# Kernel optimization log

Measured on AMD Instinct MI355X. Metric: run time of the kernel, lower is better.

## Reference

```python
import jax, jax.numpy as jnp
import numpy as np

N_NODES = 100000
N_EDGES = 1600000
N_CLASS = 10
HIDDEN = 128
BN_EPS = 1e-5


def _bn(h, gamma, beta):
    # BatchNorm1d in training mode: biased batch statistics over the node dim
    m = h.mean(axis=0)
    v = ((h - m) ** 2).mean(axis=0)
    return gamma * (h - m) / jnp.sqrt(v + BN_EPS) + beta


def _mlp(h, w1, b1, g1, t1, w2, b2, g2, t2):
    h = jax.nn.relu(_bn(h @ w1 + b1, g1, t1))
    h = jax.nn.relu(_bn(h @ w2 + b2, g2, t2))
    return h


def _gin_conv(x, edge_index, mlp_params):
    src, dst = edge_index[0], edge_index[1]
    # sum-aggregate neighbor messages: [E, D] gather + scatter-add -> [N, D]
    agg = jax.ops.segment_sum(x[src], dst, num_segments=N_NODES)
    h = x + agg  # (1 + eps) * x + agg, eps = 0
    return _mlp(h, *mlp_params)


def setup_inputs() -> dict:
    key = jax.random.key(0)
    ks = jax.random.split(key, 16)
    x = jax.random.normal(ks[0], (N_NODES, N_CLASS), dtype=jnp.float32)
    edge_index = jax.random.randint(ks[1], (2, N_EDGES), 0, N_NODES, dtype=jnp.int64)
    edge_weight = jax.random.uniform(ks[2], (N_EDGES,), dtype=jnp.float32)

    def lin(k, fan_in, fan_out):
        bound = 1.0 / np.sqrt(fan_in)
        kw, kb = jax.random.split(k)
        w = jax.random.uniform(kw, (fan_in, fan_out), minval=-bound, maxval=bound, dtype=jnp.float32)
        b = jax.random.uniform(kb, (fan_out,), minval=-bound, maxval=bound, dtype=jnp.float32)
        return w, b

    w11, b11 = lin(ks[3], N_CLASS, HIDDEN)
    w12, b12 = lin(ks[4], HIDDEN, HIDDEN)
    w21, b21 = lin(ks[5], HIDDEN, HIDDEN)
    w22, b22 = lin(ks[6], HIDDEN, HIDDEN)
    wf, bf = lin(ks[7], HIDDEN, N_CLASS)
    ones = jnp.ones((HIDDEN,), jnp.float32)
    zeros = jnp.zeros((HIDDEN,), jnp.float32)
    return {
        "x": x, "edge_weight": edge_weight,
        "w11": w11, "b11": b11, "g11": ones, "t11": zeros,
        "w12": w12, "b12": b12, "g12": ones, "t12": zeros,
        "w21": w21, "b21": b21, "g21": ones, "t21": zeros,
        "w22": w22, "b22": b22, "g22": ones, "t22": zeros,
        "wf": wf, "bf": bf,
        "edge_index": edge_index,
    }


def reference(x, edge_weight, w11, b11, g11, t11, w12, b12, g12, t12,
              w21, b21, g21, t21, w22, b22, g22, t22, wf, bf, edge_index):
    h = jax.nn.relu(_gin_conv(x, edge_index, (w11, b11, g11, t11, w12, b12, g12, t12)))
    h = jax.nn.relu(_gin_conv(h, edge_index, (w21, b21, g21, t21, w22, b22, g22, t22)))
    logits = h @ wf + bf
    return jax.nn.log_softmax(logits, axis=1)
```

## Files before the change

### kernel.cpp

```cpp
#include <hip/hip_runtime.h>

#define N_CLASS 10
#define HIDDEN 128
#define BN_EPS 1e-5f

typedef short short8 __attribute__((ext_vector_type(8)));
typedef float floatx4 __attribute__((ext_vector_type(4)));

__device__ __forceinline__ float bf2f(unsigned short u) {
    unsigned int x = ((unsigned int)u) << 16;
    float f; __builtin_memcpy(&f, &x, 4); return f;
}
__device__ __forceinline__ unsigned short f2bf(float f) {
    unsigned int x; __builtin_memcpy(&x, &f, 4);
    x += 0x7FFFu + ((x >> 16) & 1u);
    return (unsigned short)(x >> 16);
}
__device__ __forceinline__ float lo_f(unsigned int u) {
    unsigned int x = u << 16; float f; __builtin_memcpy(&f, &x, 4); return f;
}
__device__ __forceinline__ float hi_f(unsigned int u) {
    unsigned int x = u & 0xffff0000u; float f; __builtin_memcpy(&f, &x, 4); return f;
}

__global__ void hist_k(const int* __restrict__ ei, int* __restrict__ cnt,
                       int* __restrict__ rank, int E) {
    int e = blockIdx.x * 256 + threadIdx.x;
    if (e < E) rank[e] = atomicAdd(cnt + ei[E + e], 1);
}

__global__ void scanA_k(const int* __restrict__ cnt, int* __restrict__ bsum, int N) {
    __shared__ int sm[256];
    int i = blockIdx.x * 256 + threadIdx.x;
    sm[threadIdx.x] = (i < N) ? cnt[i] : 0;
    __syncthreads();
    for (int s = 128; s > 0; s >>= 1) {
        if (threadIdx.x < s) sm[threadIdx.x] += sm[threadIdx.x + s];
        __syncthreads();
    }
    if (threadIdx.x == 0) bsum[blockIdx.x] = sm[0];
}

__global__ void scanB_k(int* __restrict__ bsum, int B) {
    __shared__ int sm[512];
    int t = threadIdx.x;
    sm[t] = (t < B) ? bsum[t] : 0;
    __syncthreads();
    for (int off = 1; off < 512; off <<= 1) {
        int u = (t >= off) ? sm[t - off] : 0;
        __syncthreads();
        sm[t] += u;
        __syncthreads();
    }
    if (t < B) bsum[t] = (t == 0) ? 0 : sm[t - 1];
}

__global__ void scanC_k(const int* __restrict__ cnt, const int* __restrict__ boff,
                        int* __restrict__ row_ptr, int N) {
    __shared__ int sm[256];
    int i = blockIdx.x * 256 + threadIdx.x;
    int t = threadIdx.x;
    int v = (i < N) ? cnt[i] : 0;
    sm[t] = v;
    __syncthreads();
    for (int off = 1; off < 256; off <<= 1) {
        int u = (t >= off) ? sm[t - off] : 0;
        __syncthreads();
        sm[t] += u;
        __syncthreads();
    }
    if (i < N) row_ptr[i] = boff[blockIdx.x] + sm[t] - v;
}

__global__ void fill_k(const int* __restrict__ ei, const int* __restrict__ rank,
                       const int* __restrict__ rp, int* __restrict__ col,
                       int E, int N) {
    const int P = 4;
    const int rs = (N + P - 1) / P;
    const int stride = gridDim.x * 256;
#pragma unroll 1
    for (int pass = 0; pass < P; ++pass) {
        int lo = pass * rs, hi = lo + rs;
        for (int e = blockIdx.x * 256 + threadIdx.x; e < E; e += stride) {
            int d = ei[E + e];
            if (d >= lo && d < hi)
                col[rp[d] + rank[e]] = ei[e];
        }
    }
}

__global__ void prep_k(const float* __restrict__ W0, const float* __restrict__ W1,
                       const float* __restrict__ W2,
                       unsigned short* __restrict__ T0, unsigned short* __restrict__ T1,
                       unsigned short* __restrict__ T2,
                       float* __restrict__ stats, int* __restrict__ cnt, int N) {
    const float* W = (blockIdx.y == 0) ? W0 : (blockIdx.y == 1) ? W1 : W2;
    unsigned short* T = (blockIdx.y == 0) ? T0 : (blockIdx.y == 1) ? T1 : T2;
    int i = blockIdx.x * 256 + threadIdx.x;
    if (i < 128 * 128) {
        int k = i >> 7, n = i & 127;
        T[n * 128 + k] = f2bf(W[k * 128 + n]);
    }
    if (blockIdx.y == 0) {
        if (i < 1024) stats[i] = 0.f;
        for (int c = i; c < N; c += 64 * 256) cnt[c] = 0;
    }
}

__global__ void padx_k(const float* __restrict__ X, float* __restrict__ XP, int N) {
    int i = blockIdx.x * 256 + threadIdx.x;
    if (i >= N * 16) return;
    int node = i >> 4, f = i & 15;
    XP[i] = (f < N_CLASS) ? X[node * N_CLASS + f] : 0.f;
}

__global__ void gather10_k(const float* __restrict__ XP, const int* __restrict__ col,
                           const int* __restrict__ rp, const int* __restrict__ cnt,
                           float* __restrict__ out, int N) {
    int t = blockIdx.x * 256 + threadIdx.x;
    int node = t >> 4, f = t & 15;
    if (node >= N) return;
    int start = rp[node], deg = cnt[node];
    float acc = XP[node * 16 + f];
    int j = 0;
    for (; j + 8 <= deg; j += 8) {
        int s0 = col[start + j],     s1 = col[start + j + 1];
        int s2 = col[start + j + 2], s3 = col[start + j + 3];
        int s4 = col[start + j + 4], s5 = col[start + j + 5];
        int s6 = col[start + j + 6], s7 = col[start + j + 7];
        float v0 = XP[s0 * 16 + f];
        float v1 = XP[s1 * 16 + f];
        float v2 = XP[s2 * 16 + f];
        float v3 = XP[s3 * 16 + f];
        float v4 = XP[s4 * 16 + f];
        float v5 = XP[s5 * 16 + f];
        float v6 = XP[s6 * 16 + f];
        float v7 = XP[s7 * 16 + f];
        acc += v0; acc += v1; acc += v2; acc += v3;
        acc += v4; acc += v5; acc += v6; acc += v7;
    }
    for (; j < deg; ++j)
        acc += XP[col[start + j] * 16 + f];
    out[node * 16 + f] = acc;
}

__global__ __launch_bounds__(256) void act2_k(
    const unsigned short* __restrict__ Z, unsigned short* __restrict__ R,
    const float* __restrict__ st, const float* __restrict__ g,
    const float* __restrict__ b, int N, float inv_n) {
    __shared__ float sTab[128], hTab[128];
    int tid = threadIdx.x;
    if (tid < 128) {
        float m = st[tid] * inv_n;
        float v = fmaxf(st[128 + tid] * inv_n - m * m, 0.f);
        float s = g[tid] * rsqrtf(v + BN_EPS);
        sTab[tid] = s;
        hTab[tid] = b[tid] - m * s;
    }
    __syncthreads();
    int total = N * 16;
    for (int i = blockIdx.x * 256 + tid; i < total; i += gridDim.x * 256) {
        int k8 = (i & 15) * 8;
        uint4 v = ((const uint4*)Z)[i];
        unsigned short* us = (unsigned short*)&v;
#pragma unroll
        for (int j = 0; j < 8; ++j) {
            float f = fmaxf(fmaf(bf2f(us[j]), sTab[k8 + j], hTab[k8 + j]), 0.f);
            us[j] = f2bf(f);
        }
        ((uint4*)R)[i] = v;
    }
}

__global__ __launch_bounds__(256) void gather_sum_k(
    const unsigned short* __restrict__ R, const int* __restrict__ col,
    const int* __restrict__ rp, const int* __restrict__ cnt,
    unsigned short* __restrict__ out, int N) {
    int wave = __builtin_amdgcn_readfirstlane((blockIdx.x * 256 + threadIdx.x) >> 6);
    int lane = threadIdx.x & 63;
    if (wave >= N) return;
    int start = __builtin_amdgcn_readfirstlane(rp[wave]);
    int deg   = __builtin_amdgcn_readfirstlane(cnt[wave]);
    const unsigned int* Xv = (const unsigned int*)R;
    unsigned int self = Xv[wave * 64 + lane];
    float a0 = lo_f(self);
    float a1 = hi_f(self);
    int j = 0;
    for (; j + 8 <= deg; j += 8) {
        int n0 = col[start + j],     n1 = col[start + j + 1];
        int n2 = col[start + j + 2], n3 = col[start + j + 3];
        int n4 = col[start + j + 4], n5 = col[start + j + 5];
        int n6 = col[start + j + 6], n7 = col[start + j + 7];
        unsigned int w0 = Xv[n0 * 64 + lane];
        unsigned int w1 = Xv[n1 * 64 + lane];
        unsigned int w2 = Xv[n2 * 64 + lane];
        unsigned int w3 = Xv[n3 * 64 + lane];
        unsigned int w4 = Xv[n4 * 64 + lane];
        unsigned int w5 = Xv[n5 * 64 + lane];
        unsigned int w6 = Xv[n6 * 64 + lane];
        unsigned int w7 = Xv[n7 * 64 + lane];
        a0 += lo_f(w0); a1 += hi_f(w0);
        a0 += lo_f(w1); a1 += hi_f(w1);
        a0 += lo_f(w2); a1 += hi_f(w2);
        a0 += lo_f(w3); a1 += hi_f(w3);
        a0 += lo_f(w4); a1 += hi_f(w4);
        a0 += lo_f(w5); a1 += hi_f(w5);
        a0 += lo_f(w6); a1 += hi_f(w6);
        a0 += lo_f(w7); a1 += hi_f(w7);
    }
    for (; j < deg; ++j) {
        unsigned int v = Xv[col[start + j] * 64 + lane];
        a0 += lo_f(v); a1 += hi_f(v);
    }
    unsigned int o = (unsigned int)f2bf(a0) | ((unsigned int)f2bf(a1) << 16);
    ((unsigned int*)out)[wave * 64 + lane] = o;
}

__global__ __launch_bounds__(128) void gemm10_k(
    const float* __restrict__ A, const float* __restrict__ W,
    const float* __restrict__ bias, unsigned short* __restrict__ C,
    float* __restrict__ stOut, int N) {
    __shared__ float rb[16 * 16];
    const int tid = threadIdx.x;
    float wreg[N_CLASS];
#pragma unroll
    for (int k = 0; k < N_CLASS; ++k) wreg[k] = W[k * HIDDEN + tid];
    float bb = bias[tid];
    float s = 0.f, s2 = 0.f;
    for (int r0 = blockIdx.x * 16; r0 < N; r0 += gridDim.x * 16) {
        int nr = min(16, N - r0);
        for (int i = tid; i < nr * 16; i += 128) rb[i] = A[r0 * 16 + i];
        __syncthreads();
        for (int r = 0; r < nr; ++r) {
            float acc = bb;
#pragma unroll
            for (int k = 0; k < N_CLASS; ++k) acc = fmaf(rb[r * 16 + k], wreg[k], acc);
            C[(r0 + r) * HIDDEN + tid] = f2bf(acc);
            s += acc; s2 += acc * acc;
        }
        __syncthreads();
    }
    atomicAdd(stOut + tid, s);
    atomicAdd(stOut + HIDDEN + tid, s2);
}

template<bool BN>
__global__ __launch_bounds__(256) void gemm_mfma_k(
    const unsigned short* __restrict__ Zin, const unsigned short* __restrict__ Wt,
    const float* __restrict__ bias,
    const float* __restrict__ stIn, const float* __restrict__ gIn,
    const float* __restrict__ tIn,
    unsigned short* __restrict__ Zout, float* __restrict__ stOut,
    int N, float inv_n) {
    __shared__ unsigned short Wl[128 * 136];
    __shared__ unsigned short Al[64 * 136];
    __shared__ float sTab[128], hTab[128], biasTab[128];
    __shared__ float redS[128], redS2[128];

    const int tid  = threadIdx.x;
    const int wv   = tid >> 6;
    const int ln   = tid & 63;
    const int half = ln >> 4;
    const int l16  = ln & 15;

    if (tid < 128) {
        biasTab[tid] = bias[tid];
        if (BN) {
            float m = stIn[tid] * inv_n;
            float v = fmaxf(stIn[128 + tid] * inv_n - m * m, 0.f);
            float s = gIn[tid] * rsqrtf(v + BN_EPS);
            sTab[tid] = s;
            hTab[tid] = tIn[tid] - m * s;
        }
        redS[tid] = 0.f; redS2[tid] = 0.f;
    }
    for (int c = tid; c < 2048; c += 256) {
        int n = c >> 4, k8 = c & 15;
        uint4 v = *(const uint4*)(Wt + n * 128 + k8 * 8);
        *(uint4*)(&Wl[n * 136 + k8 * 8]) = v;
    }
    __syncthreads();

    float cs[8], cs2[8];
#pragma unroll
    for (int i = 0; i < 8; ++i) { cs[i] = 0.f; cs2[i] = 0.f; }

    const int ntiles = (N + 63) >> 6;
    for (int tile = blockIdx.x; tile < ntiles; tile += gridDim.x) {
        const int r0 = tile * 64;
        for (int c = tid; c < 1024; c += 256) {
            int r = c >> 4, k8 = c & 15;
            int gr = r0 + r; if (gr >= N) gr = N - 1;
            uint4 v = *(const uint4*)(Zin + gr * 128 + k8 * 8);
            if (BN) {
                unsigned short* us = (unsigned short*)&v;
                int kb = k8 * 8;
#pragma unroll
                for (int j = 0; j < 8; ++j) {
                    float f = fmaxf(fmaf(bf2f(us[j]), sTab[kb + j], hTab[kb + j]), 0.f);
                    us[j] = f2bf(f);
                }
            }
            *(uint4*)(&Al[r * 136 + k8 * 8]) = v;
        }
        __syncthreads();

        short8 afrag[4];
        const int arow = wv * 16 + l16;
#pragma unroll
        for (int s = 0; s < 4; ++s)
            afrag[s] = *(const short8*)(&Al[arow * 136 + s * 32 + half * 8]);
        __syncthreads();

#pragma unroll
        for (int ct = 0; ct < 8; ++ct) {
            floatx4 acc = {0.f, 0.f, 0.f, 0.f};
            const int bn_ = ct * 16 + l16;
#pragma unroll
            for (int s = 0; s < 4; ++s) {
                short8 bfrag = *(const short8*)(&Wl[bn_ * 136 + s * 32 + half * 8]);
                acc = __builtin_amdgcn_mfma_f32_16x16x32_bf16(afrag[s], bfrag, acc, 0, 0, 0);
            }
            float bcol = biasTab[bn_];
#pragma unroll
            for (int r = 0; r < 4; ++r) {
                int lrow = wv * 16 + half * 4 + r;
                float val = acc[r] + bcol;
                if (r0 + lrow < N) { cs[ct] += val; cs2[ct] += val * val; }
                Al[lrow * 136 + bn_] = f2bf(val);
            }
        }
        __syncthreads();

        for (int c = tid; c < 1024; c += 256) {
            int r = c >> 4, k8 = c & 15;
            int gr = r0 + r;
            if (gr < N)
                *(uint4*)(Zout + gr * 128 + k8 * 8) = *(const uint4*)(&Al[r * 136 + k8 * 8]);
        }
        __syncthreads();
    }

#pragma unroll
    for (int ct = 0; ct < 8; ++ct) {
        float a = cs[ct], b = cs2[ct];
        a += __shfl_xor(a, 16); a += __shfl_xor(a, 32);
        b += __shfl_xor(b, 16); b += __shfl_xor(b, 32);
        if (half == 0) {
            atomicAdd(&redS[ct * 16 + l16], a);
            atomicAdd(&redS2[ct * 16 + l16], b);
        }
    }
    __syncthreads();
    if (tid < 128) {
        atomicAdd(stOut + tid, redS[tid]);
        atomicAdd(stOut + 128 + tid, redS2[tid]);
    }
}

__global__ __launch_bounds__(256) void final_mfma_k(
    const unsigned short* __restrict__ Z, const float* __restrict__ st,
    const float* __restrict__ g, const float* __restrict__ b,
    const float* __restrict__ wf, const float* __restrict__ bfc,
    float* __restrict__ out, int N, float inv_n) {
    __shared__ unsigned short Al[64 * 136];
    __shared__ unsigned short Bl[16 * 136];
    __shared__ float sTab[128], hTab[128], biasTab[16];

    const int tid  = threadIdx.x;
    const int wv   = tid >> 6;
    const int ln   = tid & 63;
    const int half = ln >> 4;
    const int l16  = ln & 15;

    if (tid < 128) {
        float m = st[tid] * inv_n;
        float v = fmaxf(st[128 + tid] * inv_n - m * m, 0.f);
        float s = g[tid] * rsqrtf(v + BN_EPS);
        sTab[tid] = s;
        hTab[tid] = b[tid] - m * s;
    }
    if (tid < 16) biasTab[tid] = (tid < N_CLASS) ? bfc[tid] : -3.0e38f;
    {
        int n = tid >> 4, k8 = (tid & 15) * 8;
        uint4 v;
        unsigned short* us = (unsigned short*)&v;
#pragma unroll
        for (int j = 0; j < 8; ++j)
            us[j] = (n < N_CLASS) ? f2bf(wf[(k8 + j) * N_CLASS + n]) : (unsigned short)0;
        *(uint4*)(&Bl[n * 136 + k8]) = v;
    }
    __syncthreads();

    short8 bfrag[4];
#pragma unroll
    for (int s = 0; s < 4; ++s)
        bfrag[s] = *(const short8*)(&Bl[l16 * 136 + s * 32 + half * 8]);

    const int ntiles = (N + 63) >> 6;
    for (int tile = blockIdx.x; tile < ntiles; tile += gridDim.x) {
        const int r0 = tile * 64;
        for (int c = tid; c < 1024; c += 256) {
            int r = c >> 4, k8 = c & 15;
            int gr = r0 + r; if (gr >= N) gr = N - 1;
            uint4 v = *(const uint4*)(Z + gr * 128 + k8 * 8);
            unsigned short* us = (unsigned short*)&v;
            int kb = k8 * 8;
#pragma unroll
            for (int j = 0; j < 8; ++j) {
                float f = fmaxf(fmaf(bf2f(us[j]), sTab[kb + j], hTab[kb + j]), 0.f);
                us[j] = f2bf(f);
            }
            *(uint4*)(&Al[r * 136 + k8 * 8]) = v;
        }
        __syncthreads();

        short8 afrag[4];
        const int arow = wv * 16 + l16;
#pragma unroll
        for (int s = 0; s < 4; ++s)
            afrag[s] = *(const short8*)(&Al[arow * 136 + s * 32 + half * 8]);
        __syncthreads();

        floatx4 acc = {0.f, 0.f, 0.f, 0.f};
#pragma unroll
        for (int s = 0; s < 4; ++s)
            acc = __builtin_amdgcn_mfma_f32_16x16x32_bf16(afrag[s], bfrag[s], acc, 0, 0, 0);

        float bcol = biasTab[l16];
#pragma unroll
        for (int r = 0; r < 4; ++r) {
            float lg = acc[r] + bcol;
            float mx = lg;
            mx = fmaxf(mx, __shfl_xor(mx, 1));
            mx = fmaxf(mx, __shfl_xor(mx, 2));
            mx = fmaxf(mx, __shfl_xor(mx, 4));
            mx = fmaxf(mx, __shfl_xor(mx, 8));
            float p = __expf(lg - mx);
            float se = p;
            se += __shfl_xor(se, 1);
            se += __shfl_xor(se, 2);
            se += __shfl_xor(se, 4);
            se += __shfl_xor(se, 8);
            float ls = __logf(se);
            int grow = r0 + wv * 16 + half * 4 + r;
            if (l16 < N_CLASS && grow < N)
                out[grow * N_CLASS + l16] = lg - mx - ls;
        }
    }
}


extern "C" void kernel_launch(void* const* d_in, const int* in_sizes, int n_in,
                              void* d_out, int out_size, void* d_ws, size_t ws_size,
                              hipStream_t stream) {
    const float* x   = (const float*)d_in[0];
    const float* w11 = (const float*)d_in[2];
    const float* b11 = (const float*)d_in[3];
    const float* g11 = (const float*)d_in[4];
    const float* t11 = (const float*)d_in[5];
    const float* w12 = (const float*)d_in[6];
    const float* b12 = (const float*)d_in[7];
    const float* g12 = (const float*)d_in[8];
    const float* t12 = (const float*)d_in[9];
    const float* w21 = (const float*)d_in[10];
    const float* b21 = (const float*)d_in[11];
    const float* g21 = (const float*)d_in[12];
    const float* t21 = (const float*)d_in[13];
    const float* w22 = (const float*)d_in[14];
    const float* b22 = (const float*)d_in[15];
    const float* g22 = (const float*)d_in[16];
    const float* t22 = (const float*)d_in[17];
    const float* wf  = (const float*)d_in[18];
    const float* bf  = (const float*)d_in[19];
    const int*   ei  = (const int*)d_in[20];

    const int N = in_sizes[0] / N_CLASS;
    const int E = in_sizes[1];
    const float inv_n = 1.0f / (float)N;

    char* base = (char*)d_ws;
    size_t off = 0;
    auto take = [&](size_t bytes) { void* p = base + off; off += (bytes + 15) & ~(size_t)15; return p; };
    float*          stats   = (float*)take(1024 * 4);
    float*          xp      = (float*)take((size_t)N * 16 * 4);
    float*          h0      = (float*)take((size_t)N * 16 * 4);
    int*            cnt     = (int*)take((size_t)N * 4);
    int*            row_ptr = (int*)take((size_t)N * 4);
    int*            rank    = (int*)take((size_t)E * 4);
    int*            bsum    = (int*)take(512 * 4);
    int*            col     = (int*)take((size_t)E * 4);
    unsigned short* bufA    = (unsigned short*)take((size_t)N * HIDDEN * 2);
    unsigned short* bufB    = (unsigned short*)take((size_t)N * HIDDEN * 2);
    unsigned short* bufC    = (unsigned short*)take((size_t)N * HIDDEN * 2);
    unsigned short* Wt1     = (unsigned short*)take(128 * 128 * 2);
    unsigned short* Wt2     = (unsigned short*)take(128 * 128 * 2);
    unsigned short* Wt3     = (unsigned short*)take(128 * 128 * 2);

    const int nB = (N + 255) / 256;
    const int gE = (E + 255) / 256;

    prep_k<<<dim3(64, 3), 256, 0, stream>>>(w12, w21, w22, Wt1, Wt2, Wt3,
                                            stats, cnt, N);
    padx_k<<<(N * 16 + 255) / 256, 256, 0, stream>>>(x, xp, N);

    hist_k<<<gE, 256, 0, stream>>>(ei, cnt, rank, E);
    scanA_k<<<nB, 256, 0, stream>>>(cnt, bsum, N);
    scanB_k<<<1, 512, 0, stream>>>(bsum, nB);
    scanC_k<<<nB, 256, 0, stream>>>(cnt, bsum, row_ptr, N);
    fill_k<<<gE, 256, 0, stream>>>(ei, rank, row_ptr, col, E, N);

    gather10_k<<<(N * 16 + 255) / 256, 256, 0, stream>>>(xp, col, row_ptr, cnt, h0, N);
    gemm10_k<<<512, 128, 0, stream>>>(h0, w11, b11, bufA, stats, N);
    gemm_mfma_k<true><<<512, 256, 0, stream>>>(bufA, Wt1, b12, stats, g11, t11,
                                               bufB, stats + 256, N, inv_n);

    act2_k<<<3125, 256, 0, stream>>>(bufB, bufC, stats + 256, g12, t12, N, inv_n);
    gather_sum_k<<<(N * 64 + 255) / 256, 256, 0, stream>>>(bufC, col, row_ptr, cnt,
                                                           bufA, N);

    gemm_mfma_k<false><<<512, 256, 0, stream>>>(bufA, Wt2, b21, nullptr, nullptr, nullptr,
                                                bufB, stats + 512, N, inv_n);
    gemm_mfma_k<true><<<512, 256, 0, stream>>>(bufB, Wt3, b22, stats + 512, g21, t21,
                                               bufA, stats + 768, N, inv_n);

    final_mfma_k<<<782, 256, 0, stream>>>(bufA, stats + 768, g22, t22,
                                          wf, bf, (float*)d_out, N, inv_n);
}
```

Before: 434.9 us.

## Build CSR via two-level bucket sort with shared-memory atomics

```diff
diff --git a/kernel.cpp b/kernel.cpp
--- a/kernel.cpp
+++ b/kernel.cpp
@@ -23,28 +23,25 @@
     unsigned int x = u & 0xffff0000u; float f; __builtin_memcpy(&f, &x, 4); return f;
 }
 
-__global__ void hist_k(const int* __restrict__ ei, int* __restrict__ cnt,
-                       int* __restrict__ rank, int E) {
-    int e = blockIdx.x * 256 + threadIdx.x;
-    if (e < E) rank[e] = atomicAdd(cnt + ei[E + e], 1);
-}
-
-__global__ void scanA_k(const int* __restrict__ cnt, int* __restrict__ bsum, int N) {
-    __shared__ int sm[256];
-    int i = blockIdx.x * 256 + threadIdx.x;
-    sm[threadIdx.x] = (i < N) ? cnt[i] : 0;
-    __syncthreads();
-    for (int s = 128; s > 0; s >>= 1) {
-        if (threadIdx.x < s) sm[threadIdx.x] += sm[threadIdx.x + s];
-        __syncthreads();
-    }
-    if (threadIdx.x == 0) bsum[blockIdx.x] = sm[0];
-}
-
-__global__ void scanB_k(int* __restrict__ bsum, int B) {
+
+__global__ __launch_bounds__(512) void bhist_k(const int* __restrict__ ei,
+                                               int* __restrict__ bhist, int E) {
+    __shared__ int h[512];
+    int tid = threadIdx.x;
+    h[tid] = 0;
+    __syncthreads();
+    for (int e = blockIdx.x * 512 + tid; e < E; e += gridDim.x * 512)
+        atomicAdd(&h[((unsigned)ei[E + e]) >> 8], 1);
+    __syncthreads();
+    if (h[tid]) atomicAdd(&bhist[tid], h[tid]);
+}
+
+__global__ __launch_bounds__(512) void bscan_k(const int* __restrict__ bhist,
+                                               int* __restrict__ bstart,
+                                               int* __restrict__ bcur, int NBK) {
     __shared__ int sm[512];
     int t = threadIdx.x;
-    sm[t] = (t < B) ? bsum[t] : 0;
+    sm[t] = (t < NBK) ? bhist[t] : 0;
     __syncthreads();
     for (int off = 1; off < 512; off <<= 1) {
         int u = (t >= off) ? sm[t - off] : 0;
@@ -52,40 +49,67 @@
         sm[t] += u;
         __syncthreads();
     }
-    if (t < B) bsum[t] = (t == 0) ? 0 : sm[t - 1];
-}
-
-__global__ void scanC_k(const int* __restrict__ cnt, const int* __restrict__ boff,
-                        int* __restrict__ row_ptr, int N) {
-    __shared__ int sm[256];
-    int i = blockIdx.x * 256 + threadIdx.x;
-    int t = threadIdx.x;
-    int v = (i < N) ? cnt[i] : 0;
-    sm[t] = v;
+    int excl = (t == 0) ? 0 : sm[t - 1];
+    if (t <= NBK) bstart[t] = excl;
+    if (t < NBK)  bcur[t]   = excl;
+}
+
+__global__ __launch_bounds__(512) void bscatter_k(const int* __restrict__ ei,
+                                                  int* __restrict__ bcur,
+                                                  int2* __restrict__ pairs, int E) {
+    __shared__ int h[512], base[512], cur[512];
+    int tid = threadIdx.x;
+    h[tid] = 0; cur[tid] = 0;
+    __syncthreads();
+    int chunk = (E + gridDim.x - 1) / gridDim.x;
+    int e0 = blockIdx.x * chunk;
+    int e1 = min(e0 + chunk, E);
+    for (int e = e0 + tid; e < e1; e += 512)
+        atomicAdd(&h[((unsigned)ei[E + e]) >> 8], 1);
+    __syncthreads();
+    base[tid] = h[tid] ? atomicAdd(&bcur[tid], h[tid]) : 0;
+    __syncthreads();
+    for (int e = e0 + tid; e < e1; e += 512) {
+        int s = ei[e], d = ei[E + e];
+        int bk = ((unsigned)d) >> 8;
+        int r = atomicAdd(&cur[bk], 1);
+        pairs[base[bk] + r] = make_int2(s, d);
+    }
+}
+
+__global__ __launch_bounds__(512) void bcsr_k(const int2* __restrict__ pairs,
+                                              const int* __restrict__ bstart,
+                                              int* __restrict__ row_ptr,
+                                              int* __restrict__ cnt,
+                                              int* __restrict__ col, int N) {
+    __shared__ int h[256], sc[256], cur[256];
+    int tid = threadIdx.x;
+    if (tid < 256) { h[tid] = 0; cur[tid] = 0; }
+    __syncthreads();
+    int b = blockIdx.x, lo = b << 8;
+    int s = bstart[b], e = bstart[b + 1];
+    for (int i = s + tid; i < e; i += 512)
+        atomicAdd(&h[pairs[i].y - lo], 1);
+    __syncthreads();
+    if (tid < 256) sc[tid] = h[tid];
     __syncthreads();
     for (int off = 1; off < 256; off <<= 1) {
-        int u = (t >= off) ? sm[t - off] : 0;
-        __syncthreads();
-        sm[t] += u;
-        __syncthreads();
-    }
-    if (i < N) row_ptr[i] = boff[blockIdx.x] + sm[t] - v;
-}
-
-__global__ void fill_k(const int* __restrict__ ei, const int* __restrict__ rank,
-                       const int* __restrict__ rp, int* __restrict__ col,
-                       int E, int N) {
-    const int P = 4;
-    const int rs = (N + P - 1) / P;
-    const int stride = gridDim.x * 256;
-#pragma unroll 1
-    for (int pass = 0; pass < P; ++pass) {
-        int lo = pass * rs, hi = lo + rs;
-        for (int e = blockIdx.x * 256 + threadIdx.x; e < E; e += stride) {
-            int d = ei[E + e];
-            if (d >= lo && d < hi)
-                col[rp[d] + rank[e]] = ei[e];
-        }
+        int u = (tid < 256 && tid >= off) ? sc[tid - off] : 0;
+        __syncthreads();
+        if (tid < 256) sc[tid] += u;
+        __syncthreads();
+    }
+    if (tid < 256) {
+        int d = lo + tid;
+        if (d < N) { cnt[d] = h[tid]; row_ptr[d] = s + sc[tid] - h[tid]; }
+        sc[tid] -= h[tid];
+    }
+    __syncthreads();
+    for (int i = s + tid; i < e; i += 512) {
+        int2 p = pairs[i];
+        int d = p.y - lo;
+        int r = atomicAdd(&cur[d], 1);
+        col[s + sc[d] + r] = p.x;
     }
 }
 
@@ -93,7 +117,7 @@
                        const float* __restrict__ W2,
                        unsigned short* __restrict__ T0, unsigned short* __restrict__ T1,
                        unsigned short* __restrict__ T2,
-                       float* __restrict__ stats, int* __restrict__ cnt, int N) {
+                       float* __restrict__ stats, int* __restrict__ bhist) {
     const float* W = (blockIdx.y == 0) ? W0 : (blockIdx.y == 1) ? W1 : W2;
     unsigned short* T = (blockIdx.y == 0) ? T0 : (blockIdx.y == 1) ? T1 : T2;
     int i = blockIdx.x * 256 + threadIdx.x;
@@ -103,7 +127,7 @@
     }
     if (blockIdx.y == 0) {
         if (i < 1024) stats[i] = 0.f;
-        for (int c = i; c < N; c += 64 * 256) cnt[c] = 0;
+        if (i < 512)  bhist[i] = 0;
     }
 }
 
@@ -478,6 +502,7 @@
     const int N = in_sizes[0] / N_CLASS;
     const int E = in_sizes[1];
     const float inv_n = 1.0f / (float)N;
+    const int NBK = (N + 255) >> 8;
 
     char* base = (char*)d_ws;
     size_t off = 0;
@@ -487,8 +512,10 @@
     float*          h0      = (float*)take((size_t)N * 16 * 4);
     int*            cnt     = (int*)take((size_t)N * 4);
     int*            row_ptr = (int*)take((size_t)N * 4);
-    int*            rank    = (int*)take((size_t)E * 4);
-    int*            bsum    = (int*)take(512 * 4);
+    int*            bhist   = (int*)take(512 * 4);
+    int*            bstart  = (int*)take(520 * 4);
+    int*            bcur    = (int*)take(512 * 4);
+    int2*           pairs   = (int2*)take((size_t)E * 8);
     int*            col     = (int*)take((size_t)E * 4);
     unsigned short* bufA    = (unsigned short*)take((size_t)N * HIDDEN * 2);
     unsigned short* bufB    = (unsigned short*)take((size_t)N * HIDDEN * 2);
@@ -497,18 +524,14 @@
     unsigned short* Wt2     = (unsigned short*)take(128 * 128 * 2);
     unsigned short* Wt3     = (unsigned short*)take(128 * 128 * 2);
 
-    const int nB = (N + 255) / 256;
-    const int gE = (E + 255) / 256;
-
     prep_k<<<dim3(64, 3), 256, 0, stream>>>(w12, w21, w22, Wt1, Wt2, Wt3,
-                                            stats, cnt, N);
+                                            stats, bhist);
     padx_k<<<(N * 16 + 255) / 256, 256, 0, stream>>>(x, xp, N);
 
-    hist_k<<<gE, 256, 0, stream>>>(ei, cnt, rank, E);
-    scanA_k<<<nB, 256, 0, stream>>>(cnt, bsum, N);
-    scanB_k<<<1, 512, 0, stream>>>(bsum, nB);
-    scanC_k<<<nB, 256, 0, stream>>>(cnt, bsum, row_ptr, N);
-    fill_k<<<gE, 256, 0, stream>>>(ei, rank, row_ptr, col, E, N);
+    bhist_k<<<256, 512, 0, stream>>>(ei, bhist, E);
+    bscan_k<<<1, 512, 0, stream>>>(bhist, bstart, bcur, NBK);
+    bscatter_k<<<256, 512, 0, stream>>>(ei, bcur, pairs, E);
+    bcsr_k<<<NBK, 512, 0, stream>>>(pairs, bstart, row_ptr, cnt, col, N);
 
     gather10_k<<<(N * 16 + 255) / 256, 256, 0, stream>>>(xp, col, row_ptr, cnt, h0, N);
     gemm10_k<<<512, 128, 0, stream>>>(h0, w11, b11, bufA, stats, N);
```

After: 404.3 us. 1.08x faster.
